# Performance work log

Hardware: AMD Instinct MI355X
Metric: run time of the kernel (lower is better)

Reference implementation:

```python
import jax, jax.numpy as jnp
import numpy as np

B, C, H, W = 2, 256, 64, 64
D = 4  # max dilation ring


def _offsets():
    offs = [(0, 0)]
    for s in range(1, D + 1):
        for a in (-s, 0, s):
            for b in (-s, 0, s):
                if a != 0 or b != 0:
                    offs.append((a, b))
    return np.array(offs, dtype=np.int32)  # (33, 2)


def setup_inputs() -> dict:
    key = jax.random.key(0)
    k1, k2, k3, k4 = jax.random.split(key, 4)
    scale = 1.0 / np.sqrt(C)
    return {
        "Ft": jax.random.normal(k1, (B, C, H, W), dtype=jnp.float32),
        "Ft_epsilon": jax.random.normal(k2, (B, C, H, W), dtype=jnp.float32),
        "Wf": jax.random.normal(k3, (256, C), dtype=jnp.float32) * scale,
        "bf": jnp.zeros((256,), dtype=jnp.float32),
        "Wg": jax.random.normal(k4, (256, C), dtype=jnp.float32) * scale,
        "bg": jnp.zeros((256,), dtype=jnp.float32),
    }


def reference(Ft, Ft_epsilon, Wf, bf, Wg, bg):
    # 1x1 conv embeddings
    Ef = jnp.einsum("bchw,oc->bohw", Ft, Wf) + bf[None, :, None, None]          # f(Ft)
    Eg = jnp.einsum("bchw,oc->bohw", Ft_epsilon, Wg) + bg[None, :, None, None]  # g(Ft_eps)

    offs = _offsets()                                  # (K,2), K=33
    dx = jnp.asarray(offs[:, 0])[:, None, None]        # (K,1,1)
    dy = jnp.asarray(offs[:, 1])[:, None, None]
    xs = jnp.arange(H)[None, :, None] + dx             # (K,H,1)
    ys = jnp.arange(W)[None, None, :] + dy             # (K,1,W)
    valid = ((xs >= 0) & (xs < H)) & ((ys >= 0) & (ys < W))  # (K,H,W)
    xc = jnp.clip(xs, 0, H - 1)
    yc = jnp.clip(ys, 0, W - 1)

    # gather neighbor embeddings and features: (B,C,K,H,W)
    Ef_n = Ef[:, :, xc, yc]
    Ft_n = Ft[:, :, xc, yc]

    # affinity of center embedding with each neighbor embedding
    aff = jnp.einsum("bchw,bckhw->bkhw", Eg, Ef_n)     # (B,K,H,W)
    aff = jnp.where(valid[None], aff, -jnp.inf)        # clip out-of-bounds neighbors
    w = jax.nn.softmax(aff, axis=1)                    # (B,K,H,W); center always valid

    out = jnp.einsum("bkhw,bckhw->bchw", w, Ft_n)      # (B,C,H,W)
    return out
```

## Files before the change

### kernel.cpp

```cpp
#include <hip/hip_runtime.h>
#include <math.h>

typedef __attribute__((ext_vector_type(4))) float f4;

__device__ __forceinline__ int iclamp(int x, int lo, int hi) { return min(max(x, lo), hi); }

__device__ constexpr int DXS[33] = {-4,-4,-4, -3,-3,-3, -2,-2,-2, -1,-1,-1,
                                     0,0,0,0,0,0,0,0,0,
                                     1,1,1, 2,2,2, 3,3,3, 4,4,4};
__device__ constexpr int DYS[33] = {-4,0,4, -3,0,3, -2,0,2, -1,0,1,
                                    -4,-3,-2,-1,0,1,2,3,4,
                                    -1,0,1, -2,0,2, -3,0,3, -4,0,4};

__global__ __launch_bounds__(256, 1) void gemm_f32(
    const float* __restrict__ Wf, const float* __restrict__ bf,
    const float* __restrict__ Wg, const float* __restrict__ bg,
    const float* __restrict__ Ft, const float* __restrict__ FtE,
    float* __restrict__ Ef, float* __restrict__ Eg)
{
    __shared__ float As[2][16][132];
    __shared__ float Bs[2][16][128];

    const int gb = blockIdx.z;
    const int g = gb >> 1, b = gb & 1;
    const float* Wmat = g ? Wg : Wf;
    const float* bias = g ? bg : bf;
    const float* X = (g ? FtE : Ft) + (size_t)b * 256 * 4096;
    float* E = (g ? Eg : Ef) + (size_t)b * 256 * 4096;

    const int tid = threadIdx.x;
    const int tn = tid & 15, tm = tid >> 4;
    const int m0 = blockIdx.y * 128, n0 = blockIdx.x * 128;

    float acc[8][8] = {};
    f4 areg[2], breg[2];

    auto loadG = [&](int kk) {
        #pragma unroll
        for (int i = 0; i < 2; ++i) {
            int f = i * 256 + tid;
            areg[i] = *(const f4*)&Wmat[(size_t)(m0 + (f >> 2)) * 256 + kk + (f & 3) * 4];
            breg[i] = *(const f4*)&X[(size_t)(kk + (f >> 5)) * 4096 + n0 + (f & 31) * 4];
        }
    };
    auto storeL = [&](int buf) {
        #pragma unroll
        for (int i = 0; i < 2; ++i) {
            int f = i * 256 + tid;
            int o = f >> 2, cq = f & 3;
            As[buf][cq * 4 + 0][o] = areg[i].x;
            As[buf][cq * 4 + 1][o] = areg[i].y;
            As[buf][cq * 4 + 2][o] = areg[i].z;
            As[buf][cq * 4 + 3][o] = areg[i].w;
            *(f4*)&Bs[buf][f >> 5][(f & 31) * 4] = breg[i];
        }
    };

    loadG(0); storeL(0);
    __syncthreads();

    for (int ch = 0; ch < 16; ++ch) {
        const int buf = ch & 1;
        if (ch < 15) loadG((ch + 1) * 16);
        #pragma unroll
        for (int k = 0; k < 16; ++k) {
            f4 a0 = *(const f4*)&As[buf][k][tm * 8];
            f4 a1 = *(const f4*)&As[buf][k][tm * 8 + 4];
            f4 b0 = *(const f4*)&Bs[buf][k][tn * 4];
            f4 b1 = *(const f4*)&Bs[buf][k][64 + tn * 4];
            #pragma unroll
            for (int ii = 0; ii < 4; ++ii)
                #pragma unroll
                for (int jj = 0; jj < 4; ++jj) {
                    acc[ii][jj]         += a0[ii] * b0[jj];
                    acc[ii][4 + jj]     += a0[ii] * b1[jj];
                    acc[4 + ii][jj]     += a1[ii] * b0[jj];
                    acc[4 + ii][4 + jj] += a1[ii] * b1[jj];
                }
        }
        if (ch < 15) storeL(buf ^ 1);
        __syncthreads();
    }

    #pragma unroll
    for (int r = 0; r < 8; ++r) {
        int o = m0 + tm * 8 + r;
        float bvs = bias[o];
        f4 v0 = { acc[r][0] + bvs, acc[r][1] + bvs, acc[r][2] + bvs, acc[r][3] + bvs };
        f4 v1 = { acc[r][4] + bvs, acc[r][5] + bvs, acc[r][6] + bvs, acc[r][7] + bvs };
        *(f4*)&E[(size_t)o * 4096 + n0 + tn * 4] = v0;
        *(f4*)&E[(size_t)o * 4096 + n0 + 64 + tn * 4] = v1;
    }
}

__global__ __launch_bounds__(256, 1) void aff_part(
    const float* __restrict__ Ef, const float* __restrict__ Eg,
    float* __restrict__ part)
{
    __shared__ float Lef[2][4][12][72];
    __shared__ float Leg[2][4][4][64];

    const int strip = blockIdx.x, b = blockIdx.y, cseg = blockIdx.z;
    const int h0 = strip * 4, c0 = cseg * 16;
    const int tid = threadIdx.x;
    const int hs = tid >> 6, w = tid & 63;
    const int h = h0 + hs, p = h * 64 + w;
    const size_t plane = (size_t)b * 256 * 4096;
    const float* EfB = Ef + plane;
    const float* EgB = Eg + plane;

    f4 vef[3], veg; float sed[2];

    auto load_rnd = [&](int rnd) {
        const int c0r = c0 + rnd * 4;
        #pragma unroll
        for (int i = 0; i < 3; ++i) {
            int idx = i * 256 + tid;
            int ch = idx / 192, rem = idx % 192, rr = rem >> 4, c4 = rem & 15;
            int hrow = iclamp(h0 - 4 + rr, 0, 63);
            vef[i] = *(const f4*)&EfB[(size_t)(c0r + ch) * 4096 + hrow * 64 + c4 * 4];
        }
        {
            int ch = tid >> 6, rem = tid & 63, rr = rem >> 4, c4 = rem & 15;
            veg = *(const f4*)&EgB[(size_t)(c0r + ch) * 4096 + (h0 + rr) * 64 + c4 * 4];
        }
        #pragma unroll
        for (int i = 0; i < 2; ++i) {
            int e = i * 256 + tid;
            if (e < 384) {
                int row = e >> 3, sc = e & 7, ch = row / 12, rr = row % 12;
                int hrow = iclamp(h0 - 4 + rr, 0, 63);
                int wsrc = (sc < 4) ? 0 : 63;
                sed[i] = EfB[(size_t)(c0r + ch) * 4096 + hrow * 64 + wsrc];
            }
        }
    };
    auto store_rnd = [&](int buf) {
        #pragma unroll
        for (int i = 0; i < 3; ++i) {
            int idx = i * 256 + tid;
            int ch = idx / 192, rem = idx % 192, rr = rem >> 4, c4 = rem & 15;
            *(f4*)&Lef[buf][ch][rr][4 + c4 * 4] = vef[i];
        }
        {
            int ch = tid >> 6, rem = tid & 63, rr = rem >> 4, c4 = rem & 15;
            *(f4*)&Leg[buf][ch][rr][c4 * 4] = veg;
        }
        #pragma unroll
        for (int i = 0; i < 2; ++i) {
            int e = i * 256 + tid;
            if (e < 384) {
                int row = e >> 3, sc = e & 7, ch = row / 12, rr = row % 12;
                int col = (sc < 4) ? sc : (64 + sc);
                Lef[buf][ch][rr][col] = sed[i];
            }
        }
    };

    float aff[33];
    #pragma unroll
    for (int k = 0; k < 33; ++k) aff[k] = 0.f;

    load_rnd(0); store_rnd(0);
    __syncthreads();
    for (int rnd = 0; rnd < 4; ++rnd) {
        if (rnd < 3) load_rnd(rnd + 1);
        const int buf = rnd & 1;
        #pragma unroll
        for (int ch = 0; ch < 4; ++ch) {
            float eg = Leg[buf][ch][hs][w];
            #pragma unroll
            for (int k = 0; k < 33; ++k)
                aff[k] += eg * Lef[buf][ch][hs + 4 + DXS[k]][4 + w + DYS[k]];
        }
        if (rnd < 3) store_rnd(buf ^ 1);
        __syncthreads();
    }

    float* pB = part + (((size_t)cseg * 2 + b) * 33) * 4096 + p;
    #pragma unroll
    for (int k = 0; k < 33; ++k) pB[(size_t)k * 4096] = aff[k];
}

__global__ __launch_bounds__(64, 1) void softmax_k(
    const float* __restrict__ part, float* __restrict__ wgt)
{
    const int id = blockIdx.x * 64 + threadIdx.x;
    const int b = id >> 12, p = id & 4095;
    const int h = p >> 6, w = p & 63;

    float a[33];
    float m = -INFINITY;
    #pragma unroll
    for (int k = 0; k < 33; ++k) {
        float s = 0.f;
        #pragma unroll
        for (int seg = 0; seg < 16; ++seg)
            s += part[(((size_t)seg * 2 + b) * 33 + k) * 4096 + p];
        bool valid = ((unsigned)(h + DXS[k]) < 64u) && ((unsigned)(w + DYS[k]) < 64u);
        a[k] = valid ? s : -INFINITY;
        m = fmaxf(m, a[k]);
    }
    float ssum = 0.f;
    #pragma unroll
    for (int k = 0; k < 33; ++k) { float e = __expf(a[k] - m); a[k] = e; ssum += e; }
    float inv = 1.0f / ssum;
    float* wgtB = wgt + (size_t)b * 33 * 4096 + p;
    #pragma unroll
    for (int k = 0; k < 33; ++k) wgtB[(size_t)k * 4096] = a[k] * inv;
}

__global__ __launch_bounds__(256, 1) void out_kernel(
    const float* __restrict__ wgt, const float* __restrict__ Ft,
    float* __restrict__ out)
{
    __shared__ float Lft[2][4][12][72];

    const int strip = blockIdx.x, b = blockIdx.y, cseg = blockIdx.z;
    const int h0 = strip * 4, c0 = cseg * 16;
    const int tid = threadIdx.x;
    const int hs = tid >> 6, w = tid & 63;
    const int h = h0 + hs, p = h * 64 + w;
    const size_t plane = (size_t)b * 256 * 4096;
    const float* FtB = Ft + plane;
    float* outB = out + plane;

    const float* wgtB = wgt + (size_t)b * 33 * 4096 + p;
    float wv[33];
    #pragma unroll
    for (int k = 0; k < 33; ++k) wv[k] = wgtB[(size_t)k * 4096];

    f4 vef[3]; float sed[2];

    auto load_rnd = [&](int rnd) {
        const int c0r = c0 + rnd * 4;
        #pragma unroll
        for (int i = 0; i < 3; ++i) {
            int idx = i * 256 + tid;
            int ch = idx / 192, rem = idx % 192, rr = rem >> 4, c4 = rem & 15;
            int hrow = iclamp(h0 - 4 + rr, 0, 63);
            vef[i] = *(const f4*)&FtB[(size_t)(c0r + ch) * 4096 + hrow * 64 + c4 * 4];
        }
        #pragma unroll
        for (int i = 0; i < 2; ++i) {
            int e = i * 256 + tid;
            if (e < 384) {
                int row = e >> 3, sc = e & 7, ch = row / 12, rr = row % 12;
                int hrow = iclamp(h0 - 4 + rr, 0, 63);
                int wsrc = (sc < 4) ? 0 : 63;
                sed[i] = FtB[(size_t)(c0r + ch) * 4096 + hrow * 64 + wsrc];
            }
        }
    };
    auto store_rnd = [&](int buf) {
        #pragma unroll
        for (int i = 0; i < 3; ++i) {
            int idx = i * 256 + tid;
            int ch = idx / 192, rem = idx % 192, rr = rem >> 4, c4 = rem & 15;
            *(f4*)&Lft[buf][ch][rr][4 + c4 * 4] = vef[i];
        }
        #pragma unroll
        for (int i = 0; i < 2; ++i) {
            int e = i * 256 + tid;
            if (e < 384) {
                int row = e >> 3, sc = e & 7, ch = row / 12, rr = row % 12;
                int col = (sc < 4) ? sc : (64 + sc);
                Lft[buf][ch][rr][col] = sed[i];
            }
        }
    };

    load_rnd(0); store_rnd(0);
    __syncthreads();
    for (int rnd = 0; rnd < 4; ++rnd) {
        if (rnd < 3) load_rnd(rnd + 1);
        const int buf = rnd & 1;
        #pragma unroll
        for (int ch = 0; ch < 4; ++ch) {
            float o = 0.f;
            #pragma unroll
            for (int k = 0; k < 33; ++k)
                o += wv[k] * Lft[buf][ch][hs + 4 + DXS[k]][4 + w + DYS[k]];
            outB[(size_t)(c0 + rnd * 4 + ch) * 4096 + p] = o;
        }
        if (rnd < 3) store_rnd(buf ^ 1);
        __syncthreads();
    }
}

extern "C" void kernel_launch(void* const* d_in, const int* in_sizes, int n_in,
                              void* d_out, int out_size, void* d_ws, size_t ws_size,
                              hipStream_t stream) {
    const float* Ft  = (const float*)d_in[0];
    const float* FtE = (const float*)d_in[1];
    const float* Wf  = (const float*)d_in[2];
    const float* bf  = (const float*)d_in[3];
    const float* Wg  = (const float*)d_in[4];
    const float* bg  = (const float*)d_in[5];
    float* out = (float*)d_out;

    float* Ef  = (float*)d_ws;
    float* Eg  = Ef + (size_t)2 * 256 * 4096;
    float* part = Eg + (size_t)2 * 256 * 4096;
    float* wgt = part + (size_t)16 * 2 * 33 * 4096;

    hipLaunchKernelGGL(gemm_f32, dim3(32, 2, 4), dim3(256), 0, stream,
                       Wf, bf, Wg, bg, Ft, FtE, Ef, Eg);
    hipLaunchKernelGGL(aff_part, dim3(16, 2, 16), dim3(256), 0, stream,
                       Ef, Eg, part);
    hipLaunchKernelGGL(softmax_k, dim3(128), dim3(64), 0, stream,
                       part, wgt);
    hipLaunchKernelGGL(out_kernel, dim3(16, 2, 16), dim3(256), 0, stream,
                       wgt, Ft, out);
}
```

Baseline: 152.9 us.

## Split GEMM reduction dimension in two and sum partials in affinity kernel

The 1x1-conv GEMM now splits its K dimension across two block groups, doubling the grid from 256 to 512 blocks so more of the GPU's compute units are busy. Each group writes a separate partial Ef/Eg buffer, and the bias is added only by the first group. The affinity kernel loads both partial buffers and sums them while staging into shared memory. In exchange, the embeddings cost twice the global write and read traffic, and the workspace grows.

```diff
diff --git a/kernel.cpp b/kernel.cpp
--- a/kernel.cpp
+++ b/kernel.cpp
@@ -21,16 +21,18 @@
     __shared__ float As[2][16][132];
     __shared__ float Bs[2][16][128];
 
-    const int gb = blockIdx.z;
+    const int z = blockIdx.z;
+    const int gb = z & 3, kz = z >> 2;
     const int g = gb >> 1, b = gb & 1;
     const float* Wmat = g ? Wg : Wf;
     const float* bias = g ? bg : bf;
     const float* X = (g ? FtE : Ft) + (size_t)b * 256 * 4096;
-    float* E = (g ? Eg : Ef) + (size_t)b * 256 * 4096;
+    float* E = (g ? Eg : Ef) + (size_t)kz * 2 * 256 * 4096 + (size_t)b * 256 * 4096;
 
     const int tid = threadIdx.x;
     const int tn = tid & 15, tm = tid >> 4;
     const int m0 = blockIdx.y * 128, n0 = blockIdx.x * 128;
+    const int k0 = kz * 128;
 
     float acc[8][8] = {};
     f4 areg[2], breg[2];
@@ -56,12 +58,12 @@
         }
     };
 
-    loadG(0); storeL(0);
+    loadG(k0); storeL(0);
     __syncthreads();
 
-    for (int ch = 0; ch < 16; ++ch) {
+    for (int ch = 0; ch < 8; ++ch) {
         const int buf = ch & 1;
-        if (ch < 15) loadG((ch + 1) * 16);
+        if (ch < 7) loadG(k0 + (ch + 1) * 16);
         #pragma unroll
         for (int k = 0; k < 16; ++k) {
             f4 a0 = *(const f4*)&As[buf][k][tm * 8];
@@ -78,14 +80,14 @@
                     acc[4 + ii][4 + jj] += a1[ii] * b1[jj];
                 }
         }
-        if (ch < 15) storeL(buf ^ 1);
+        if (ch < 7) storeL(buf ^ 1);
         __syncthreads();
     }
 
     #pragma unroll
     for (int r = 0; r < 8; ++r) {
         int o = m0 + tm * 8 + r;
-        float bvs = bias[o];
+        float bvs = (kz == 0) ? bias[o] : 0.f;
         f4 v0 = { acc[r][0] + bvs, acc[r][1] + bvs, acc[r][2] + bvs, acc[r][3] + bvs };
         f4 v1 = { acc[r][4] + bvs, acc[r][5] + bvs, acc[r][6] + bvs, acc[r][7] + bvs };
         *(f4*)&E[(size_t)o * 4096 + n0 + tn * 4] = v0;
@@ -106,10 +108,13 @@
     const int hs = tid >> 6, w = tid & 63;
     const int h = h0 + hs, p = h * 64 + w;
     const size_t plane = (size_t)b * 256 * 4096;
-    const float* EfB = Ef + plane;
-    const float* EgB = Eg + plane;
-
-    f4 vef[3], veg; float sed[2];
+    const size_t half = (size_t)2 * 256 * 4096;
+    const float* Ef0 = Ef + plane;
+    const float* Ef1 = Ef + half + plane;
+    const float* Eg0 = Eg + plane;
+    const float* Eg1 = Eg + half + plane;
+
+    f4 vef0[3], vef1[3], veg0, veg1; float sed0[2], sed1[2];
 
     auto load_rnd = [&](int rnd) {
         const int c0r = c0 + rnd * 4;
@@ -118,11 +123,15 @@
             int idx = i * 256 + tid;
             int ch = idx / 192, rem = idx % 192, rr = rem >> 4, c4 = rem & 15;
             int hrow = iclamp(h0 - 4 + rr, 0, 63);
-            vef[i] = *(const f4*)&EfB[(size_t)(c0r + ch) * 4096 + hrow * 64 + c4 * 4];
+            size_t off = (size_t)(c0r + ch) * 4096 + hrow * 64 + c4 * 4;
+            vef0[i] = *(const f4*)&Ef0[off];
+            vef1[i] = *(const f4*)&Ef1[off];
         }
         {
             int ch = tid >> 6, rem = tid & 63, rr = rem >> 4, c4 = rem & 15;
-            veg = *(const f4*)&EgB[(size_t)(c0r + ch) * 4096 + (h0 + rr) * 64 + c4 * 4];
+            size_t off = (size_t)(c0r + ch) * 4096 + (h0 + rr) * 64 + c4 * 4;
+            veg0 = *(const f4*)&Eg0[off];
+            veg1 = *(const f4*)&Eg1[off];
         }
         #pragma unroll
         for (int i = 0; i < 2; ++i) {
@@ -131,7 +140,9 @@
                 int row = e >> 3, sc = e & 7, ch = row / 12, rr = row % 12;
                 int hrow = iclamp(h0 - 4 + rr, 0, 63);
                 int wsrc = (sc < 4) ? 0 : 63;
-                sed[i] = EfB[(size_t)(c0r + ch) * 4096 + hrow * 64 + wsrc];
+                size_t off = (size_t)(c0r + ch) * 4096 + hrow * 64 + wsrc;
+                sed0[i] = Ef0[off];
+                sed1[i] = Ef1[off];
             }
         }
     };
@@ -140,11 +151,13 @@
         for (int i = 0; i < 3; ++i) {
             int idx = i * 256 + tid;
             int ch = idx / 192, rem = idx % 192, rr = rem >> 4, c4 = rem & 15;
-            *(f4*)&Lef[buf][ch][rr][4 + c4 * 4] = vef[i];
+            f4 s = vef0[i] + vef1[i];
+            *(f4*)&Lef[buf][ch][rr][4 + c4 * 4] = s;
         }
         {
             int ch = tid >> 6, rem = tid & 63, rr = rem >> 4, c4 = rem & 15;
-            *(f4*)&Leg[buf][ch][rr][c4 * 4] = veg;
+            f4 s = veg0 + veg1;
+            *(f4*)&Leg[buf][ch][rr][c4 * 4] = s;
         }
         #pragma unroll
         for (int i = 0; i < 2; ++i) {
@@ -152,7 +165,7 @@
             if (e < 384) {
                 int row = e >> 3, sc = e & 7, ch = row / 12, rr = row % 12;
                 int col = (sc < 4) ? sc : (64 + sc);
-                Lef[buf][ch][rr][col] = sed[i];
+                Lef[buf][ch][rr][col] = sed0[i] + sed1[i];
             }
         }
     };
@@ -300,11 +313,11 @@
     float* out = (float*)d_out;
 
     float* Ef  = (float*)d_ws;
-    float* Eg  = Ef + (size_t)2 * 256 * 4096;
-    float* part = Eg + (size_t)2 * 256 * 4096;
+    float* Eg  = Ef + (size_t)2 * 2 * 256 * 4096;
+    float* part = Eg + (size_t)2 * 2 * 256 * 4096;
     float* wgt = part + (size_t)16 * 2 * 33 * 4096;
 
-    hipLaunchKernelGGL(gemm_f32, dim3(32, 2, 4), dim3(256), 0, stream,
+    hipLaunchKernelGGL(gemm_f32, dim3(32, 2, 8), dim3(256), 0, stream,
                        Wf, bf, Wg, bg, Ft, FtE, Ef, Eg);
     hipLaunchKernelGGL(aff_part, dim3(16, 2, 16), dim3(256), 0, stream,
                        Ef, Eg, part);
```

Result: slower. 158.7 us (+3.8%).
